# Optimization experiments

Measured on AMD Instinct MI355X. Metric: run time of the kernel, lower is better.

The kernel has to match this reference:

```python
import jax, jax.numpy as jnp
import numpy as np

B, S, IN = 1024, 256, 64
H, NT, HORIZON = 512, 8, 24


def _cell(xt, h, c, Wih, Whh, b):
    # PyTorch LSTM gate order: i, f, g, o
    g = xt @ Wih.T + h @ Whh.T + b
    i, f, gg, o = jnp.split(g, 4, axis=-1)
    c = jax.nn.sigmoid(f) * c + jax.nn.sigmoid(i) * jnp.tanh(gg)
    h = jax.nn.sigmoid(o) * jnp.tanh(c)
    return h, c


def setup_inputs() -> dict:
    key = jax.random.key(0)
    ks = jax.random.split(key, 12)
    s = 0.05
    f32 = jnp.float32
    return {
        "x": jax.random.normal(ks[0], (B, S, IN), dtype=f32),
        # encoder layer 0 / 1 (b = b_ih + b_hh folded into one vector)
        "Wih0e": jax.random.normal(ks[1], (4 * H, IN), dtype=f32) * s,
        "Whh0e": jax.random.normal(ks[2], (4 * H, H), dtype=f32) * s,
        "b0e": jnp.zeros((4 * H,), dtype=f32),
        "Wih1e": jax.random.normal(ks[3], (4 * H, H), dtype=f32) * s,
        "Whh1e": jax.random.normal(ks[4], (4 * H, H), dtype=f32) * s,
        "b1e": jnp.zeros((4 * H,), dtype=f32),
        # decoder layer 0 / 1
        "Wih0d": jax.random.normal(ks[5], (4 * H, NT), dtype=f32) * s,
        "Whh0d": jax.random.normal(ks[6], (4 * H, H), dtype=f32) * s,
        "b0d": jnp.zeros((4 * H,), dtype=f32),
        "Wih1d": jax.random.normal(ks[7], (4 * H, H), dtype=f32) * s,
        "Whh1d": jax.random.normal(ks[8], (4 * H, H), dtype=f32) * s,
        "b1d": jnp.zeros((4 * H,), dtype=f32),
        # output projection
        "Wfc": jax.random.normal(ks[9], (NT, H), dtype=f32) * s,
        "bfc": jnp.zeros((NT,), dtype=f32),
    }


def reference(x, Wih0e, Whh0e, b0e, Wih1e, Whh1e, b1e,
              Wih0d, Whh0d, b0d, Wih1d, Whh1d, b1d, Wfc, bfc):
    b = x.shape[0]
    h = Whh0e.shape[1]
    nt = Wfc.shape[0]
    z = jnp.zeros((b, h), dtype=x.dtype)

    def enc_step(carry, xt):
        h0, c0, h1, c1 = carry
        h0, c0 = _cell(xt, h0, c0, Wih0e, Whh0e, b0e)
        h1, c1 = _cell(h0, h1, c1, Wih1e, Whh1e, b1e)
        return (h0, c0, h1, c1), None

    (h0, c0, h1, c1), _ = jax.lax.scan(enc_step, (z, z, z, z), jnp.swapaxes(x, 0, 1))

    dec_in0 = jnp.zeros((b, nt), dtype=x.dtype)

    def dec_step(carry, _):
        h0, c0, h1, c1, di = carry
        h0, c0 = _cell(di, h0, c0, Wih0d, Whh0d, b0d)
        h1, c1 = _cell(h0, h1, c1, Wih1d, Whh1d, b1d)
        out = h1 @ Wfc.T + bfc  # fed back as next decoder input
        return (h0, c0, h1, c1, out), out

    _, outs = jax.lax.scan(dec_step, (h0, c0, h1, c1, dec_in0), None, length=HORIZON)
    return jnp.swapaxes(outs, 0, 1)  # (batch, horizon, num_tickers)
```

## Files before the change

kernel.cpp:

```cpp
#include <hip/hip_runtime.h>


typedef _Float16 half_t;
typedef _Float16 half8 __attribute__((ext_vector_type(8)));
typedef float floatx4 __attribute__((ext_vector_type(4)));
typedef unsigned long long u64;
typedef u64 u64x2 __attribute__((ext_vector_type(2)));

#define B_ 1024
#define S_ 256
#define IN_ 64
#define H_ 512
#define NT_ 8
#define HOR_ 24
#define NG_ 2048
#define BH_ (B_ * H_)
#define FIDX(s, mm) ((((s) * 16) + (mm)) << 5)

__device__ __forceinline__ void async_cp16(const void* g, void* l) {
  __builtin_amdgcn_global_load_lds((const __attribute__((address_space(1))) void*)g,
                                   (__attribute__((address_space(3))) void*)l,
                                   16, 0, 0);
}

__device__ __forceinline__ float fast_sig(float x) {
  return __builtin_amdgcn_rcpf(1.0f + __builtin_amdgcn_exp2f(-1.44269504f * x));
}
__device__ __forceinline__ float fast_tanh(float x) {
  float xx = fminf(10.0f, fmaxf(-10.0f, x));
  float e = __builtin_amdgcn_exp2f(2.88539008f * xx);
  return (e - 1.0f) * __builtin_amdgcn_rcpf(e + 1.0f);
}

__device__ __forceinline__ u64 sys_ld8(const void* p) {
  return __hip_atomic_load((const u64*)p, __ATOMIC_RELAXED, __HIP_MEMORY_SCOPE_SYSTEM);
}
__device__ __forceinline__ unsigned sys_ld4(const void* p) {
  return __hip_atomic_load((const unsigned*)p, __ATOMIC_RELAXED, __HIP_MEMORY_SCOPE_SYSTEM);
}
__device__ __forceinline__ void sys_st8(void* p, u64 v) {
  __hip_atomic_store((u64*)p, v, __ATOMIC_RELAXED, __HIP_MEMORY_SCOPE_SYSTEM);
}
__device__ __forceinline__ void sys_st4(void* p, unsigned v) {
  __hip_atomic_store((unsigned*)p, v, __ATOMIC_RELAXED, __HIP_MEMORY_SCOPE_SYSTEM);
}
__device__ __forceinline__ void wait_ge(const int* f, int tgt) {
  while (__hip_atomic_load(f, __ATOMIC_RELAXED, __HIP_MEMORY_SCOPE_SYSTEM) < tgt)
    __builtin_amdgcn_s_sleep(1);
  asm volatile("" ::: "memory");
}
__device__ __forceinline__ void bump(int* f) {
  asm volatile("" ::: "memory");
  __hip_atomic_fetch_add(f, 1, __ATOMIC_RELAXED, __HIP_MEMORY_SCOPE_SYSTEM);
  asm volatile("" ::: "memory");
}


__global__ void k_xT(const float* __restrict__ x, half_t* __restrict__ xf) {
  int i = blockIdx.x * 256 + threadIdx.x;
  int e = i & 63;
  int tb = i >> 6;
  int t = tb >> 10;
  int b = tb & 1023;
  xf[i] = (half_t)x[((size_t)b * S_ + t) * 64 + e];
}

__global__ void k_pack(const float* __restrict__ Wih, const float* __restrict__ Whh,
                       const float* __restrict__ bias,
                       half_t* __restrict__ Wp, float* __restrict__ bp,
                       int K0real, int K0pad, int K) {
  int i = blockIdx.x * 256 + threadIdx.x;
  if (i >= NG_ * K) return;
  int r = i / K;
  int k = i - r * K;
  int j = r >> 2, g = r & 3;
  int src = g * H_ + j;
  float v;
  if (k < K0pad) v = (k < K0real) ? Wih[src * K0real + k] : 0.0f;
  else           v = Whh[src * H_ + (k - K0pad)];
  Wp[i] = (half_t)v;
  if (k == 0) bp[r] = bias[src];
}

__global__ void k_init(half_t* h0, half_t* h1, half_t* dpad,
                       int* fh0, int* fh1, int* ffc) {
  int i = blockIdx.x * 256 + threadIdx.x;
  if (i < BH_) {
    h0[i] = (half_t)0.0f; h0[i + BH_] = (half_t)0.0f; h0[i + 2 * BH_] = (half_t)0.0f;
    h1[i] = (half_t)0.0f; h1[i + BH_] = (half_t)0.0f; h1[i + 2 * BH_] = (half_t)0.0f;
  }
  if (i < B_ * 64) dpad[i] = (half_t)0.0f;
  if (i < 384 * 16) {
    int v = (i < 32) ? 16 : 0;
    fh0[i << 5] = v; fh1[i << 5] = v;
  }
  if (i < 32 * 16) ffc[i << 5] = 0;
}


__device__ __forceinline__ void gemm_cell(
    half_t* ldsA, half_t* ldsB, half_t* ldsH, bool mode0, bool sysA0,
    const half_t* s0, int str0, const half_t* sA, const half_t* sB,
    const half_t* __restrict__ Bs, int K, int NC,
    const float* __restrict__ bp, float* creg,
    half_t* __restrict__ hout, int M0, int N0) {
  const int tid = threadIdx.x;
  const int l = tid & 63, w = tid >> 6;
  const int wm = w >> 1, wn = w & 1;
  const int fr = l & 15, q = l >> 4;
  const int r8 = l >> 3, c8 = l & 7;

  floatx4 acc[2][4];
#pragma unroll
  for (int a = 0; a < 2; ++a)
#pragma unroll
    for (int b = 0; b < 4; ++b) acc[a][b] = (floatx4){0.f, 0.f, 0.f, 0.f};

  auto issue_A = [&](int c, u64 (&ar)[2][2]) {
    const half_t* base; int str; bool sys;
    if (mode0) {
      if (c == 0) { base = s0; str = str0; sys = sysA0; }
      else        { base = sA + (size_t)(c - 1) * 64; str = H_; sys = true; }
    } else {
      base = (c < 8) ? sA + (size_t)c * 64 : sB + (size_t)(c - 8) * 64;
      str = H_; sys = true;
    }
#pragma unroll
    for (int ii = 0; ii < 2; ++ii) {
      int i = 2 * w + ii;
      int r = 8 * i + r8;
      int sc = c8 ^ r8;
      const half_t* p = base + (size_t)r * str + sc * 8;
      if (sys) {
        ar[ii][0] = sys_ld8(p);
        ar[ii][1] = sys_ld8(p + 4);
      } else {
        ar[ii][0] = ((const u64*)p)[0];
        ar[ii][1] = ((const u64*)p)[1];
      }
    }
  };
  auto write_A = [&](int buf, u64 (&ar)[2][2]) {
    half_t* la = ldsA + buf * 4096;
#pragma unroll
    for (int ii = 0; ii < 2; ++ii) {
      int i = 2 * w + ii;
      u64x2 v = {ar[ii][0], ar[ii][1]};
      *(u64x2*)(la + i * 512 + 64 * r8 + 8 * c8) = v;
    }
  };
  auto stage_B = [&](int c, int buf) {
    half_t* lb = ldsB + buf * 8192;
    const half_t* bsrc = Bs + (size_t)c * 64;
#pragma unroll
    for (int jj = 0; jj < 4; ++jj) {
      int j = 4 * w + jj;
      int r = 8 * j + r8;
      int sc = c8 ^ r8;
      async_cp16(bsrc + (size_t)r * K + sc * 8, lb + j * 512);
    }
  };

  u64 ar[2][2][2];
  issue_A(0, ar[0]);
  write_A(0, ar[0]);
  stage_B(0, 0);
  issue_A(1, ar[1]);
  int buf = 0;
  for (int c = 0; c < NC; ++c) {
    __syncthreads();
    if (c + 2 < NC) issue_A(c + 2, ar[c & 1]);
    if (c + 1 < NC) {
      write_A(buf ^ 1, ar[(c + 1) & 1]);
      stage_B(c + 1, buf ^ 1);
    }
    const half_t* la = ldsA + buf * 4096;
    const half_t* lb = ldsB + buf * 8192;
#pragma unroll
    for (int kk = 0; kk < 2; ++kk) {
      half8 av[2], bv[4];
#pragma unroll
      for (int mt = 0; mt < 2; ++mt) {
        int r = wm * 32 + mt * 16 + fr;
        int sc = (4 * kk + q) ^ (fr & 7);
        av[mt] = *(const half8*)(la + r * 64 + sc * 8);
      }
#pragma unroll
      for (int nt = 0; nt < 4; ++nt) {
        int r = wn * 64 + nt * 16 + fr;
        int sc = (4 * kk + q) ^ (fr & 7);
        bv[nt] = *(const half8*)(lb + r * 64 + sc * 8);
      }
#pragma unroll
      for (int mt = 0; mt < 2; ++mt)
#pragma unroll
        for (int nt = 0; nt < 4; ++nt)
          acc[mt][nt] = __builtin_amdgcn_mfma_f32_16x16x32_f16(av[mt], bv[nt], acc[mt][nt], 0, 0, 0);
    }
    buf ^= 1;
  }

  const int base = l & ~3;
  const int gsel = l & 3;
#pragma unroll
  for (int nt = 0; nt < 4; ++nt) {
    const int ncl = wn * 64 + nt * 16 + fr;
    const float bc = bp[N0 + ncl];
    const int lc = ncl >> 2;
#pragma unroll
    for (int mt = 0; mt < 2; ++mt) {
      const float csnap = creg[nt * 2 + mt];
#pragma unroll
      for (int r = 0; r < 4; ++r) {
        float v = acc[mt][nt][r] + bc;
        float gi = __shfl(v, base + 0);
        float gf = __shfl(v, base + 1);
        float gg = __shfl(v, base + 2);
        float go = __shfl(v, base + 3);
        float cold = __shfl(csnap, base + r);
        const float cn = fast_sig(gf) * cold + fast_sig(gi) * fast_tanh(gg);
        const float hn = fast_sig(go) * fast_tanh(cn);
        if (gsel == r) creg[nt * 2 + mt] = cn;
        if (gsel == 0) {
          const int lm = wm * 32 + mt * 16 + q * 4 + r;
          ldsH[lm * 32 + lc] = (half_t)hn;
        }
      }
    }
  }
  __syncthreads();
  {
    const int tr = tid >> 2, cg = tid & 3;
    const u64* lp = (const u64*)(ldsH + tr * 32 + cg * 8);
    half_t* dst = hout + (size_t)(M0 + tr) * H_ + (N0 >> 2) + cg * 8;
    sys_st8(dst, lp[0]);
    sys_st8(dst + 4, lp[1]);
    u64 ca = sys_ld8(dst);
    u64 cb = sys_ld8(dst + 4);
    asm volatile("" :: "v"(ca), "v"(cb));
  }
}


__global__ __launch_bounds__(256, 2)
void k_seq(const half_t* __restrict__ xf,
           const half_t* __restrict__ Wp0e, const float* __restrict__ bp0e,
           const half_t* __restrict__ Wp1e, const float* __restrict__ bp1e,
           const half_t* __restrict__ Wp0d, const float* __restrict__ bp0d,
           const half_t* __restrict__ Wp1d, const float* __restrict__ bp1d,
           half_t* __restrict__ h0, half_t* __restrict__ h1,
           half_t* __restrict__ dpad,
           const float* __restrict__ Wfc, const float* __restrict__ bfc,
           float* __restrict__ out,
           int* __restrict__ fh0, int* __restrict__ fh1, int* __restrict__ ffc) {
  __shared__ __align__(16) half_t ldsA[2 * 64 * 64];
  __shared__ __align__(16) half_t ldsB[2 * 128 * 64];
  __shared__ __align__(16) half_t ldsH[64 * 32];

  const int tid = threadIdx.x;
  const int bid = blockIdx.x;
  const int wtype = bid >> 8;
  const int b8 = bid & 255;
  const int n = 2 * (b8 & 7) + ((b8 >> 3) & 1);
  const int m = b8 >> 4;
  const int M0 = m * 64, N0 = n * 128;

  half_t* h0s[3] = {h0, h0 + BH_, h0 + 2 * BH_};
  half_t* h1s[3] = {h1, h1 + BH_, h1 + 2 * BH_};

  float cr[8];
#pragma unroll
  for (int i = 0; i < 8; ++i) cr[i] = 0.0f;

  if (wtype == 0) {
    for (int u = 0; u < S_ + HOR_; ++u) {
      const bool dec = (u >= S_);
      const int t = u - S_;
      if (tid == 0) {
        wait_ge(fh0 + FIDX(u + 1, m), 16);
        if (u >= 1) wait_ge(fh1 + FIDX(u - 1, m), 16);
        if (dec && t >= 1) wait_ge(ffc + FIDX(t - 1, m), 1);
      }
      __syncthreads();
      asm volatile("" ::: "memory");
      const int scur = u % 3, sp = (u + 2) % 3;
      gemm_cell(ldsA, ldsB, ldsH, true, dec,
                dec ? (dpad + (size_t)M0 * 64)
                    : (xf + ((size_t)u * B_ + M0) * 64), 64,
                h0s[sp] + (size_t)M0 * H_, (const half_t*)0,
                (dec ? Wp0d : Wp0e) + (size_t)N0 * 576, 576, 9,
                dec ? bp0d : bp0e, cr, h0s[scur], M0, N0);
      __syncthreads();
      if (tid == 0) bump(fh0 + FIDX(u + 2, m));
    }
  } else {
    for (int u = 0; u < S_ + HOR_; ++u) {
      const bool dec = (u >= S_);
      const int t = u - S_;
      if (tid == 0) {
        wait_ge(fh0 + FIDX(u + 2, m), 16);
        wait_ge(fh1 + FIDX(u + 1, m), 16);
        if (u >= S_ + 3) wait_ge(ffc + FIDX(u - S_ - 3, m), 1);
      }
      __syncthreads();
      asm volatile("" ::: "memory");
      const int scur = u % 3, sp = (u + 2) % 3;
      gemm_cell(ldsA, ldsB, ldsH, false, false, (const half_t*)0, 0,
                h0s[scur] + (size_t)M0 * H_, h1s[sp] + (size_t)M0 * H_,
                (dec ? Wp1d : Wp1e) + (size_t)N0 * 1024, 1024, 16,
                dec ? bp1d : bp1e, cr, h1s[scur], M0, N0);
      __syncthreads();
      if (tid == 0) bump(fh1 + FIDX(u + 2, m));
      if (dec && n == 0) {
        if (tid == 0) wait_ge(fh1 + FIDX(u + 2, m), 16);
        __syncthreads();
        asm volatile("" ::: "memory");
        for (int half = 0; half < 2; ++half) {
#pragma unroll
          for (int i = 0; i < 16; ++i) {
            int li = tid * 16 + i;
            int rr = li >> 7, ee = li & 127;
            ((u64*)ldsB)[li] =
                sys_ld8(h1s[scur] + (size_t)(M0 + half * 32 + rr) * H_ + ee * 4);
          }
          __syncthreads();
          const int r = tid >> 3, cc = tid & 7;
          const int rowg = M0 + half * 32 + r;
          const half_t* hl = ldsB + r * 512;
          const float* wr = Wfc + cc * H_;
          float s = bfc[cc];
#pragma unroll 8
          for (int k8 = 0; k8 < H_ / 8; ++k8) {
            half8 hv = *(const half8*)(hl + k8 * 8);
#pragma unroll
            for (int e = 0; e < 8; ++e) s += (float)hv[e] * wr[k8 * 8 + e];
          }
          out[((size_t)rowg * HOR_ + t) * NT_ + cc] = s;
          float sn = __shfl(s, (tid & 63) + 1);
          if (!(cc & 1)) {
            half_t* dp = dpad + rowg * 64 + cc;
            unsigned pk = (unsigned)__builtin_bit_cast(unsigned short, (half_t)s)
                        | ((unsigned)__builtin_bit_cast(unsigned short, (half_t)sn) << 16);
            sys_st4(dp, pk);
            unsigned ck = sys_ld4(dp);
            asm volatile("" :: "v"(ck));
          }
          __syncthreads();
        }
        if (tid == 0) bump(ffc + FIDX(t, m));
      }
    }
  }
}


extern "C" void kernel_launch(void* const* d_in, const int* in_sizes, int n_in,
                              void* d_out, int out_size, void* d_ws, size_t ws_size,
                              hipStream_t stream) {
  (void)in_sizes; (void)n_in; (void)out_size; (void)ws_size;
  const float* x     = (const float*)d_in[0];
  const float* Wih0e = (const float*)d_in[1];
  const float* Whh0e = (const float*)d_in[2];
  const float* b0e   = (const float*)d_in[3];
  const float* Wih1e = (const float*)d_in[4];
  const float* Whh1e = (const float*)d_in[5];
  const float* b1e   = (const float*)d_in[6];
  const float* Wih0d = (const float*)d_in[7];
  const float* Whh0d = (const float*)d_in[8];
  const float* b0d   = (const float*)d_in[9];
  const float* Wih1d = (const float*)d_in[10];
  const float* Whh1d = (const float*)d_in[11];
  const float* b1d   = (const float*)d_in[12];
  const float* Wfc   = (const float*)d_in[13];
  const float* bfc   = (const float*)d_in[14];
  float* out = (float*)d_out;

  char* p = (char*)d_ws;
  auto alloc = [&](size_t bytes) {
    char* r = p;
    p += (bytes + 255) & ~(size_t)255;
    return r;
  };
  half_t* xf   = (half_t*)alloc((size_t)S_ * B_ * 64 * 2);
  half_t* Wp0e = (half_t*)alloc((size_t)NG_ * 576 * 2);
  half_t* Wp1e = (half_t*)alloc((size_t)NG_ * 1024 * 2);
  half_t* Wp0d = (half_t*)alloc((size_t)NG_ * 576 * 2);
  half_t* Wp1d = (half_t*)alloc((size_t)NG_ * 1024 * 2);
  float*  bp0e = (float*)alloc(NG_ * 4);
  float*  bp1e = (float*)alloc(NG_ * 4);
  float*  bp0d = (float*)alloc(NG_ * 4);
  float*  bp1d = (float*)alloc(NG_ * 4);
  half_t* h0   = (half_t*)alloc((size_t)3 * BH_ * 2);
  half_t* h1   = (half_t*)alloc((size_t)3 * BH_ * 2);
  half_t* dpad = (half_t*)alloc((size_t)B_ * 64 * 2);
  int*    fh0  = (int*)alloc((size_t)384 * 16 * 32 * 4);
  int*    fh1  = (int*)alloc((size_t)384 * 16 * 32 * 4);
  int*    ffc  = (int*)alloc((size_t)32 * 16 * 32 * 4);

  k_xT<<<(S_ * B_ * 64) / 256, 256, 0, stream>>>(x, xf);
  k_pack<<<(NG_ * 576) / 256, 256, 0, stream>>>(Wih0e, Whh0e, b0e, Wp0e, bp0e, 64, 64, 576);
  k_pack<<<(NG_ * 1024) / 256, 256, 0, stream>>>(Wih1e, Whh1e, b1e, Wp1e, bp1e, 512, 512, 1024);
  k_pack<<<(NG_ * 576) / 256, 256, 0, stream>>>(Wih0d, Whh0d, b0d, Wp0d, bp0d, 8, 64, 576);
  k_pack<<<(NG_ * 1024) / 256, 256, 0, stream>>>(Wih1d, Whh1d, b1d, Wp1d, bp1d, 512, 512, 1024);
  k_init<<<BH_ / 256, 256, 0, stream>>>(h0, h1, dpad, fh0, fh1, ffc);

  k_seq<<<512, 256, 0, stream>>>(xf, Wp0e, bp0e, Wp1e, bp1e, Wp0d, bp0d, Wp1d, bp1d,
                                 h0, h1, dpad, Wfc, bfc, out, fh0, fh1, ffc);
}
```

Baseline: 7.949 ms.

## Stage recurrent hidden-state tiles per XCC via leader block copies

```diff
diff --git a/kernel.cpp b/kernel.cpp
--- a/kernel.cpp
+++ b/kernel.cpp
@@ -16,6 +16,8 @@
 #define NG_ 2048
 #define BH_ (B_ * H_)
 #define FIDX(s, mm) ((((s) * 16) + (mm)) << 5)
+#define STG0_SZ (64 * 512)
+#define STG1_SZ (64 * 1024)
 
 __device__ __forceinline__ void async_cp16(const void* g, void* l) {
   __builtin_amdgcn_global_load_lds((const __attribute__((address_space(1))) void*)g,
@@ -43,6 +45,24 @@
 }
 __device__ __forceinline__ void sys_st4(void* p, unsigned v) {
   __hip_atomic_store((unsigned*)p, v, __ATOMIC_RELAXED, __HIP_MEMORY_SCOPE_SYSTEM);
+}
+__device__ __forceinline__ u64x2 ld16_sys(const void* p) {
+  u64x2 r;
+  asm volatile("global_load_dwordx4 %0, %1, off sc0 sc1" : "=v"(r) : "v"(p));
+  return r;
+}
+__device__ __forceinline__ u64x2 ld16_sc0(const void* p) {
+  u64x2 r;
+  asm volatile("global_load_dwordx4 %0, %1, off sc0" : "=v"(r) : "v"(p));
+  return r;
+}
+__device__ __forceinline__ void vmwait0() {
+  asm volatile("s_waitcnt vmcnt(0)" ::: "memory");
+}
+__device__ __forceinline__ int get_xcc() {
+  int x;
+  asm volatile("s_getreg_b32 %0, hwreg(HW_REG_XCC_ID)" : "=s"(x));
+  return x & 7;
 }
 __device__ __forceinline__ void wait_ge(const int* f, int tgt) {
   while (__hip_atomic_load(f, __ATOMIC_RELAXED, __HIP_MEMORY_SCOPE_SYSTEM) < tgt)
@@ -83,7 +103,7 @@
 }
 
 __global__ void k_init(half_t* h0, half_t* h1, half_t* dpad,
-                       int* fh0, int* fh1, int* ffc) {
+                       int* fh0, int* fh1, int* ffc, int* rdy, int* xccmap) {
   int i = blockIdx.x * 256 + threadIdx.x;
   if (i < BH_) {
     h0[i] = (half_t)0.0f; h0[i + BH_] = (half_t)0.0f; h0[i + 2 * BH_] = (half_t)0.0f;
@@ -95,9 +115,12 @@
     fh0[i << 5] = v; fh1[i << 5] = v;
   }
   if (i < 32 * 16) ffc[i << 5] = 0;
-}
-
-
+  if (i < 128) rdy[i << 5] = 0;
+  if (i < 512) xccmap[i << 5] = -1;
+}
+
+
+template <bool SC0A>
 __device__ __forceinline__ void gemm_cell(
     half_t* ldsA, half_t* ldsB, half_t* ldsH, bool mode0, bool sysA0,
     const half_t* s0, int str0, const half_t* sA, const half_t* sB,
@@ -116,14 +139,14 @@
 #pragma unroll
     for (int b = 0; b < 4; ++b) acc[a][b] = (floatx4){0.f, 0.f, 0.f, 0.f};
 
-  auto issue_A = [&](int c, u64 (&ar)[2][2]) {
-    const half_t* base; int str; bool sys;
+  auto issue_A = [&](int c, u64x2 (&ar)[2]) {
+    const half_t* base; int str; int flavor;
     if (mode0) {
-      if (c == 0) { base = s0; str = str0; sys = sysA0; }
-      else        { base = sA + (size_t)(c - 1) * 64; str = H_; sys = true; }
+      if (c == 0) { base = s0; str = str0; flavor = sysA0 ? 1 : 0; }
+      else        { base = sA + (size_t)(c - 1) * 64; str = H_; flavor = 2; }
     } else {
       base = (c < 8) ? sA + (size_t)c * 64 : sB + (size_t)(c - 8) * 64;
-      str = H_; sys = true;
+      str = H_; flavor = 2;
     }
 #pragma unroll
     for (int ii = 0; ii < 2; ++ii) {
@@ -131,22 +154,17 @@
       int r = 8 * i + r8;
       int sc = c8 ^ r8;
       const half_t* p = base + (size_t)r * str + sc * 8;
-      if (sys) {
-        ar[ii][0] = sys_ld8(p);
-        ar[ii][1] = sys_ld8(p + 4);
-      } else {
-        ar[ii][0] = ((const u64*)p)[0];
-        ar[ii][1] = ((const u64*)p)[1];
-      }
+      if (flavor == 0)      ar[ii] = *(const u64x2*)p;
+      else if (flavor == 1) ar[ii] = ld16_sys(p);
+      else                  ar[ii] = SC0A ? ld16_sc0(p) : ld16_sys(p);
     }
   };
-  auto write_A = [&](int buf, u64 (&ar)[2][2]) {
+  auto write_A = [&](int buf, u64x2 (&ar)[2]) {
     half_t* la = ldsA + buf * 4096;
 #pragma unroll
     for (int ii = 0; ii < 2; ++ii) {
       int i = 2 * w + ii;
-      u64x2 v = {ar[ii][0], ar[ii][1]};
-      *(u64x2*)(la + i * 512 + 64 * r8 + 8 * c8) = v;
+      *(u64x2*)(la + i * 512 + 64 * r8 + 8 * c8) = ar[ii];
     }
   };
   auto stage_B = [&](int c, int buf) {
@@ -161,8 +179,9 @@
     }
   };
 
-  u64 ar[2][2][2];
+  u64x2 ar[2][2];
   issue_A(0, ar[0]);
+  vmwait0();
   write_A(0, ar[0]);
   stage_B(0, 0);
   issue_A(1, ar[1]);
@@ -252,21 +271,68 @@
            half_t* __restrict__ dpad,
            const float* __restrict__ Wfc, const float* __restrict__ bfc,
            float* __restrict__ out,
-           int* __restrict__ fh0, int* __restrict__ fh1, int* __restrict__ ffc) {
+           int* __restrict__ fh0, int* __restrict__ fh1, int* __restrict__ ffc,
+           half_t* __restrict__ stg0, half_t* __restrict__ stg1,
+           int* __restrict__ rdy, int* __restrict__ xccmap) {
   __shared__ __align__(16) half_t ldsA[2 * 64 * 64];
   __shared__ __align__(16) half_t ldsB[2 * 128 * 64];
   __shared__ __align__(16) half_t ldsH[64 * 32];
+  __shared__ int s_flag;
 
   const int tid = threadIdx.x;
   const int bid = blockIdx.x;
   const int wtype = bid >> 8;
   const int b8 = bid & 255;
-  const int n = 2 * (b8 & 7) + ((b8 >> 3) & 1);
-  const int m = b8 >> 4;
+  const int x   = b8 & 7;
+  const int idx = b8 >> 3;
+  const int j   = idx & 3;
+  const int mm  = idx >> 2;
+  const int n   = (2 * x + j) & 15;
+  const int m   = mm + 8 * (x & 1);
   const int M0 = m * 64, N0 = n * 128;
+  const bool leader = (j == 0);
+  const int leader_bid = wtype * 256 + x + 32 * mm;
+  const int slotbase = x * 8 + mm;
+  int* rdyp = rdy + ((wtype * 64 + slotbase) << 5);
 
   half_t* h0s[3] = {h0, h0 + BH_, h0 + 2 * BH_};
   half_t* h1s[3] = {h1, h1 + BH_, h1 + 2 * BH_};
+
+  const int phys = get_xcc();
+  if (tid == 0) {
+    sys_st4(xccmap + (bid << 5), (unsigned)phys);
+    unsigned rb = sys_ld4(xccmap + (bid << 5));
+    asm volatile("" :: "v"(rb));
+  }
+  bool useStage = true;
+  if (!leader) {
+    if (tid == 0) {
+      unsigned lx;
+      while ((lx = sys_ld4(xccmap + (leader_bid << 5))) == 0xFFFFFFFFu)
+        __builtin_amdgcn_s_sleep(1);
+      s_flag = (lx == (unsigned)phys) ? 1 : 0;
+    }
+    __syncthreads();
+    useStage = (s_flag != 0);
+    asm volatile("" ::: "memory");
+  }
+
+  auto copy_rounds = [&](const half_t* __restrict__ src, half_t* __restrict__ dst) {
+    for (int g = 0; g < 16; g += 8) {
+      u64x2 v[8];
+#pragma unroll
+      for (int i2 = 0; i2 < 8; ++i2) {
+        int off = ((g + i2) * 256 + tid) * 8;
+        v[i2] = ld16_sys(src + off);
+      }
+      vmwait0();
+#pragma unroll
+      for (int i2 = 0; i2 < 8; ++i2) {
+        int off = ((g + i2) * 256 + tid) * 8;
+        *((u64x2*)(dst + off)) = v[i2];
+      }
+    }
+  };
 
   float cr[8];
 #pragma unroll
@@ -284,12 +350,32 @@
       __syncthreads();
       asm volatile("" ::: "memory");
       const int scur = u % 3, sp = (u + 2) % 3;
-      gemm_cell(ldsA, ldsB, ldsH, true, dec,
-                dec ? (dpad + (size_t)M0 * 64)
-                    : (xf + ((size_t)u * B_ + M0) * 64), 64,
-                h0s[sp] + (size_t)M0 * H_, (const half_t*)0,
-                (dec ? Wp0d : Wp0e) + (size_t)N0 * 576, 576, 9,
-                dec ? bp0d : bp0e, cr, h0s[scur], M0, N0);
+      const half_t* s0 = dec ? (dpad + (size_t)M0 * 64)
+                             : (xf + ((size_t)u * B_ + M0) * 64);
+      const half_t* srcA = h0s[sp] + (size_t)M0 * H_;
+      const half_t* W = (dec ? Wp0d : Wp0e) + (size_t)N0 * 576;
+      const float* bpp = dec ? bp0d : bp0e;
+      half_t* stgA = stg0 + (size_t)((u & 1) * 64 + slotbase) * STG0_SZ;
+      if (leader) {
+        copy_rounds(srcA, stgA);
+        __syncthreads();
+        if (tid == 0)
+          __hip_atomic_store(rdyp, u + 1, __ATOMIC_RELAXED, __HIP_MEMORY_SCOPE_AGENT);
+        gemm_cell<true>(ldsA, ldsB, ldsH, true, dec, s0, 64,
+                        stgA, (const half_t*)0, W, 576, 9, bpp, cr, h0s[scur], M0, N0);
+      } else if (useStage) {
+        if (tid == 0) {
+          while (__hip_atomic_load(rdyp, __ATOMIC_RELAXED, __HIP_MEMORY_SCOPE_AGENT) < u + 1)
+            __builtin_amdgcn_s_sleep(1);
+        }
+        __syncthreads();
+        asm volatile("" ::: "memory");
+        gemm_cell<true>(ldsA, ldsB, ldsH, true, dec, s0, 64,
+                        stgA, (const half_t*)0, W, 576, 9, bpp, cr, h0s[scur], M0, N0);
+      } else {
+        gemm_cell<false>(ldsA, ldsB, ldsH, true, dec, s0, 64,
+                         srcA, (const half_t*)0, W, 576, 9, bpp, cr, h0s[scur], M0, N0);
+      }
       __syncthreads();
       if (tid == 0) bump(fh0 + FIDX(u + 2, m));
     }
@@ -305,10 +391,33 @@
       __syncthreads();
       asm volatile("" ::: "memory");
       const int scur = u % 3, sp = (u + 2) % 3;
-      gemm_cell(ldsA, ldsB, ldsH, false, false, (const half_t*)0, 0,
-                h0s[scur] + (size_t)M0 * H_, h1s[sp] + (size_t)M0 * H_,
-                (dec ? Wp1d : Wp1e) + (size_t)N0 * 1024, 1024, 16,
-                dec ? bp1d : bp1e, cr, h1s[scur], M0, N0);
+      const half_t* srcA = h0s[scur] + (size_t)M0 * H_;
+      const half_t* srcB = h1s[sp] + (size_t)M0 * H_;
+      const half_t* W = (dec ? Wp1d : Wp1e) + (size_t)N0 * 1024;
+      const float* bpp = dec ? bp1d : bp1e;
+      half_t* stgA = stg1 + (size_t)((u & 1) * 64 + slotbase) * STG1_SZ;
+      half_t* stgB = stgA + 64 * 512;
+      if (leader) {
+        copy_rounds(srcA, stgA);
+        copy_rounds(srcB, stgB);
+        __syncthreads();
+        if (tid == 0)
+          __hip_atomic_store(rdyp, u + 1, __ATOMIC_RELAXED, __HIP_MEMORY_SCOPE_AGENT);
+        gemm_cell<true>(ldsA, ldsB, ldsH, false, false, (const half_t*)0, 0,
+                        stgA, stgB, W, 1024, 16, bpp, cr, h1s[scur], M0, N0);
+      } else if (useStage) {
+        if (tid == 0) {
+          while (__hip_atomic_load(rdyp, __ATOMIC_RELAXED, __HIP_MEMORY_SCOPE_AGENT) < u + 1)
+            __builtin_amdgcn_s_sleep(1);
+        }
+        __syncthreads();
+        asm volatile("" ::: "memory");
+        gemm_cell<true>(ldsA, ldsB, ldsH, false, false, (const half_t*)0, 0,
+                        stgA, stgB, W, 1024, 16, bpp, cr, h1s[scur], M0, N0);
+      } else {
+        gemm_cell<false>(ldsA, ldsB, ldsH, false, false, (const half_t*)0, 0,
+                         srcA, srcB, W, 1024, 16, bpp, cr, h1s[scur], M0, N0);
+      }
       __syncthreads();
       if (tid == 0) bump(fh1 + FIDX(u + 2, m));
       if (dec && n == 0) {
@@ -396,14 +505,19 @@
   int*    fh0  = (int*)alloc((size_t)384 * 16 * 32 * 4);
   int*    fh1  = (int*)alloc((size_t)384 * 16 * 32 * 4);
   int*    ffc  = (int*)alloc((size_t)32 * 16 * 32 * 4);
+  half_t* stg0 = (half_t*)alloc((size_t)2 * 64 * STG0_SZ * 2);
+  half_t* stg1 = (half_t*)alloc((size_t)2 * 64 * STG1_SZ * 2);
+  int*    rdy  = (int*)alloc((size_t)128 * 32 * 4);
+  int*    xccm = (int*)alloc((size_t)512 * 32 * 4);
 
   k_xT<<<(S_ * B_ * 64) / 256, 256, 0, stream>>>(x, xf);
   k_pack<<<(NG_ * 576) / 256, 256, 0, stream>>>(Wih0e, Whh0e, b0e, Wp0e, bp0e, 64, 64, 576);
   k_pack<<<(NG_ * 1024) / 256, 256, 0, stream>>>(Wih1e, Whh1e, b1e, Wp1e, bp1e, 512, 512, 1024);
   k_pack<<<(NG_ * 576) / 256, 256, 0, stream>>>(Wih0d, Whh0d, b0d, Wp0d, bp0d, 8, 64, 576);
   k_pack<<<(NG_ * 1024) / 256, 256, 0, stream>>>(Wih1d, Whh1d, b1d, Wp1d, bp1d, 512, 512, 1024);
-  k_init<<<BH_ / 256, 256, 0, stream>>>(h0, h1, dpad, fh0, fh1, ffc);
+  k_init<<<BH_ / 256, 256, 0, stream>>>(h0, h1, dpad, fh0, fh1, ffc, rdy, xccm);
 
   k_seq<<<512, 256, 0, stream>>>(xf, Wp0e, bp0e, Wp1e, bp1e, Wp0d, bp0d, Wp1d, bp1d,
-                                 h0, h1, dpad, Wfc, bfc, out, fh0, fh1, ffc);
-}
+                                 h0, h1, dpad, Wfc, bfc, out, fh0, fh1, ffc,
+                                 stg0, stg1, rdy, xccm);
+}
```

After: 9.272 ms. 16.6% more time.
